# Kernel optimization log

Measured on AMD Instinct MI355X. Metric: run time of the kernel, lower is better.

## Reference

```python
import jax, jax.numpy as jnp
import numpy as np

NPX = 128      # nPxPup
FOV = 512      # fovInPixel = 2*samp*nPxPup, samp=2
NMODES = 54    # len(jModes)
BATCH = 8
ALPHA = np.pi / 2


def _make_consts():
    # circular pupil on the nPxPup grid
    x = np.linspace(-1.0, 1.0, NPX)
    X, Y = np.meshgrid(x, x)
    pupil = ((X ** 2 + Y ** 2) <= 1.0).astype(np.float32)
    # 4-faced pyramid phase mask on the FOV grid, pre-fftshifted
    f = np.arange(FOV) - FOV / 2
    FX, FY = np.meshgrid(f, f)
    pyr_phase = ALPHA * (np.abs(FX) + np.abs(FY))
    pyr_mask = np.fft.fftshift(np.exp(-1j * pyr_phase)).astype(np.complex64)
    return pupil, pyr_mask


def setup_inputs() -> dict:
    key = jax.random.key(0)
    k1, k2 = jax.random.split(key)
    pupil_np, mask_np = _make_consts()
    pupil = jnp.asarray(pupil_np)                      # [NPX,NPX] float32
    pyrMask = jnp.asarray(mask_np)                     # [FOV,FOV] complex64 (fftshifted)
    # Zernike-like mode basis restricted to the pupil, column-major modes as in the torch buffer
    modes = jax.random.normal(k1, (NPX * NPX, NMODES), dtype=jnp.float32) * pupil.reshape(-1, 1)
    OL1 = (jnp.eye(NMODES, dtype=jnp.float32) * 0.1)   # learnable parameter
    inputs = jax.random.normal(k2, (BATCH, 1, NPX, NPX), dtype=jnp.float32) * pupil
    return {"inputs": inputs, "modes": modes, "OL1": OL1, "pupil": pupil, "pyrMask": pyrMask}


def _prop(phase, pupil, pyrMask):
    """Vanilla pyramid WFS propagation (modulation=0).
    phase: [B,1,NPX,NPX] -> intensity [B,1,FOV,FOV]."""
    u = (pupil * jnp.exp(1j * phase)).astype(jnp.complex64)
    npv = (FOV - NPX) // 2
    field = jnp.zeros(phase.shape[:2] + (FOV, FOV), dtype=jnp.complex64)
    field = field.at[:, :, npv:npv + NPX, npv:npv + NPX].set(u)
    buf = jnp.fft.fft2(field) * pyrMask          # focal plane * pyramid mask
    return jnp.abs(jnp.fft.fft2(buf)) ** 2       # detector intensity


def reference(inputs, modes, OL1, pupil, pyrMask):
    n_modes = OL1.shape[0]
    optModes = modes @ OL1                                     # [NPX*NPX, M]
    # reference (flat wavefront) intensity
    flat = (jnp.ones((NPX, NPX), jnp.float32) * (pupil > 0))[None, None]
    I0 = _prop(flat, pupil, pyrMask)
    I0 = I0 / jnp.sum(I0)                                      # [1,1,FOV,FOV]
    gainRow = jnp.sum(OL1, axis=1)                             # [M]
    # batch the per-mode +/- push-pull propagations in one FFT pass
    zim = optModes.T.reshape(n_modes, 1, NPX, NPX)
    phases = jnp.concatenate([zim, -zim], axis=0)              # [2M,1,NPX,NPX]
    I4 = _prop(phases, pupil, pyrMask)
    I4 = I4 / jnp.sum(I4, axis=(1, 2, 3), keepdims=True)
    sp = I4[:n_modes] - I0
    sm = I4[n_modes:] - I0
    MZc = 0.5 * (sp - sm) / gainRow[:, None, None, None]
    IM = MZc.reshape(n_modes, -1).T                            # [FOV*FOV, M]
    CM = jnp.linalg.pinv(IM)                                   # [M, FOV*FOV]
    # measurement
    Ip = _prop(inputs, pupil, pyrMask)                         # [B,1,FOV,FOV]
    Inorm = jnp.sum(Ip, axis=(1, 2, 3), keepdims=True)
    Ip = Ip / Inorm - I0
    y = CM @ Ip.reshape(Ip.shape[0], -1).T                     # [M, B]
    return y
```

## Files before the change

kernel.cpp:

```cpp
#include <hip/hip_runtime.h>
#include <math.h>

#define NPIXK 262144
#define ROWF2 584

__device__ __forceinline__ int padi8(int i) { return i + (i >> 3); }
__device__ __forceinline__ int padi(int i) { return i + (i >> 5); }

#define WSYNC asm volatile("s_waitcnt lgkmcnt(0)" ::: "memory")

__device__ __forceinline__ float2 cmul(float2 a, float2 b) {
    return make_float2(a.x * b.x - a.y * b.y, a.x * b.y + a.y * b.x);
}

__device__ __forceinline__ void twchain(float ang, float2 tw[8]) {
    float s, c;
    sincosf(ang, &s, &c);
    float2 w1 = make_float2(c, s);
    float2 w2 = cmul(w1, w1);
    float2 w4 = cmul(w2, w2);
    tw[1] = w1;
    tw[2] = w2;
    tw[3] = cmul(w1, w2);
    tw[4] = w4;
    tw[5] = cmul(w1, w4);
    tw[6] = cmul(w2, w4);
    tw[7] = cmul(tw[3], w4);
}

__device__ __forceinline__ void fft8f(float vr[8], float vi[8]) {
    float er[4], ei[4], orr[4], oi[4];
    {
        float t0r = vr[0] + vr[4], t0i = vi[0] + vi[4];
        float t1r = vr[0] - vr[4], t1i = vi[0] - vi[4];
        float t2r = vr[2] + vr[6], t2i = vi[2] + vi[6];
        float t3r = vi[2] - vi[6], t3i = vr[6] - vr[2];
        er[0] = t0r + t2r; ei[0] = t0i + t2i;
        er[1] = t1r + t3r; ei[1] = t1i + t3i;
        er[2] = t0r - t2r; ei[2] = t0i - t2i;
        er[3] = t1r - t3r; ei[3] = t1i - t3i;
    }
    {
        float t0r = vr[1] + vr[5], t0i = vi[1] + vi[5];
        float t1r = vr[1] - vr[5], t1i = vi[1] - vi[5];
        float t2r = vr[3] + vr[7], t2i = vi[3] + vi[7];
        float t3r = vi[3] - vi[7], t3i = vr[7] - vr[3];
        orr[0] = t0r + t2r; oi[0] = t0i + t2i;
        orr[1] = t1r + t3r; oi[1] = t1i + t3i;
        orr[2] = t0r - t2r; oi[2] = t0i - t2i;
        orr[3] = t1r - t3r; oi[3] = t1i - t3i;
    }
    const float c = 0.70710678118654752440f;
    vr[0] = er[0] + orr[0]; vi[0] = ei[0] + oi[0];
    vr[4] = er[0] - orr[0]; vi[4] = ei[0] - oi[0];
    float t1r = c * (orr[1] + oi[1]), t1i = c * (oi[1] - orr[1]);
    vr[1] = er[1] + t1r; vi[1] = ei[1] + t1i;
    vr[5] = er[1] - t1r; vi[5] = ei[1] - t1i;
    float t2r = oi[2], t2i = -orr[2];
    vr[2] = er[2] + t2r; vi[2] = ei[2] + t2i;
    vr[6] = er[2] - t2r; vi[6] = ei[2] - t2i;
    float t3r = c * (oi[3] - orr[3]), t3i = -c * (orr[3] + oi[3]);
    vr[3] = er[3] + t3r; vi[3] = ei[3] + t3i;
    vr[7] = er[3] - t3r; vi[7] = ei[3] - t3i;
}

__device__ __forceinline__ void fft8_s34(float vr[8], float vi[8]) {
    const float c = 0.70710678118654752440f;
    float x3r = vr[3], x3i = vi[3], x4r = vr[4], x4i = vi[4];
    float A = c * (x3r + x3i), B = c * (x3r - x3i);
    vr[0] = x3r + x4r; vi[0] = x3i + x4i;
    vr[1] = -B - x4r;  vi[1] = -A - x4i;
    vr[2] = x4r - x3i; vi[2] = x3r + x4i;
    vr[3] = A - x4r;   vi[3] = -B - x4i;
    vr[4] = x4r - x3r; vi[4] = x4i - x3i;
    vr[5] = B - x4r;   vi[5] = A - x4i;
    vr[6] = x3i + x4r; vi[6] = x4i - x3r;
    vr[7] = -A - x4r;  vi[7] = B - x4i;
}

template <int SPARSE>
__device__ __forceinline__ void fft512v(float2* L, int t,
                                        float vr[8], float vi[8]) {
    if (SPARSE) fft8_s34(vr, vi); else fft8f(vr, vi);
    {
        float2* wb = L + 9 * t;
#pragma unroll
        for (int r = 0; r < 8; ++r) wb[r] = make_float2(vr[r], vi[r]);
    }
    float2 tw[8];
    twchain((float)(t & 7) * -0.09817477042468103870f, tw);
    WSYNC;
    {
        const float2* rb = L + t + (t >> 3);
        { float2 a = rb[0]; vr[0] = a.x; vi[0] = a.y; }
#pragma unroll
        for (int r = 1; r < 8; ++r) {
            float2 a = rb[72 * r];
            float2 w = tw[r];
            vr[r] = a.x * w.x - a.y * w.y;
            vi[r] = a.x * w.y + a.y * w.x;
        }
        fft8f(vr, vi);
        WSYNC;
        float2* wb = L + 9 * t;
#pragma unroll
        for (int r = 0; r < 8; ++r) wb[r] = make_float2(vr[r], vi[r]);
    }
    twchain((float)t * -0.01227184630308512985f, tw);
    WSYNC;
    {
        const float2* rb = L + 9 * (t & 7) + (t >> 3);
        { float2 a = rb[0]; vr[0] = a.x; vi[0] = a.y; }
#pragma unroll
        for (int r = 1; r < 8; ++r) {
            float2 a = rb[72 * r];
            float2 w = tw[r];
            vr[r] = a.x * w.x - a.y * w.y;
            vi[r] = a.x * w.y + a.y * w.x;
        }
        fft8f(vr, vi);
    }
}

#define FFT_LDS __shared__ float2 lds[4][ROWF2];

__device__ __forceinline__ double lsx(int i) {
    if (i == 127) return 1.0;
    return __dadd_rn(__dmul_rn((double)i, 2.0 / 127.0), -1.0);
}
__device__ __forceinline__ double pupilAt(int r, int c) {
    double xc = lsx(c), xr = lsx(r);
    double s = __dadd_rn(__dmul_rn(xc, xc), __dmul_rn(xr, xr));
    return (s <= 1.0) ? 1.0 : 0.0;
}

__global__ __launch_bounds__(256, 8) void k_s1(const float* __restrict__ optT,
                                               const float* __restrict__ inputs,
                                               float2* __restrict__ T1, int giBase) {
    FFT_LDS
    int tid = threadIdx.x, w = tid >> 6, t = tid & 63;
    int r = (blockIdx.x & 31) * 4 + w;
    int im = blockIdx.x >> 5;
    int gi = (giBase >= 0) ? giBase + im : ((im == 0) ? 0 : 108 + im);

    float vr[8], vi[8];
#pragma unroll
    for (int q = 0; q < 8; ++q) { vr[q] = 0.f; vi[q] = 0.f; }
#pragma unroll
    for (int h = 0; h < 2; ++h) {
        int c = t + 64 * h;
        int p = r * 128 + c;
        float pu = (float)pupilAt(r, c);
        float ph;
        if (gi == 0) {
            ph = pu;
        } else if (gi < 109) {
            ph = optT[(gi - 1) * 16384 + p];
        } else {
            ph = inputs[(gi - 109) * 16384 + p];
        }
        float s, cs; sincosf(ph, &s, &cs);
        vr[3 + h] = pu * cs; vi[3 + h] = pu * s;
    }
    fft512v<1>(lds[w], t, vr, vi);
    WSYNC;
#pragma unroll
    for (int q = 0; q < 8; ++q) {
        int d = t + 64 * q;
        lds[w][padi8(d)] = make_float2(vr[q], vi[q]);
    }
    __syncthreads();
    int r0 = (blockIdx.x & 31) * 4;
    float2* dst = T1 + (size_t)im * 65536;
#pragma unroll
    for (int it = 0; it < 8; ++it) {
        int g = it * 256 + tid;
        int l = g >> 2, rr = g & 3;
        dst[(size_t)l * 128 + r0 + rr] = lds[rr][padi8(l)];
    }
}

__global__ __launch_bounds__(256, 8) void k_s23(const float2* __restrict__ T1,
                                                float2* __restrict__ C2p) {
    FFT_LDS
    int tid = threadIdx.x, w = tid >> 6, t = tid & 63;
    int imgL = blockIdx.x >> 7, l = (blockIdx.x & 127) * 4 + w;
    const float2* src = T1 + (size_t)imgL * 65536 + (size_t)l * 128;
    float vr[8], vi[8];
#pragma unroll
    for (int q = 0; q < 8; ++q) { vr[q] = 0.f; vi[q] = 0.f; }
    float2 a0 = src[t], a1 = src[t + 64];
    vr[3] = a0.x; vi[3] = a0.y;
    vr[4] = a1.x; vi[4] = a1.y;
    fft512v<1>(lds[w], t, vr, vi);
    int gl = (l <= 256) ? l : 512 - l;
    int l0 = (blockIdx.x & 127) * 4;
#pragma unroll
    for (int q = 0; q < 8; ++q) {
        int k = t + 64 * q;
        int gk = (k <= 256) ? k : 512 - k;
        int n = (gk + gl) & 3;
        float a = vr[q], b = vi[q], X, Y;
        if (n == 0)      { X = a;  Y = b;  }
        else if (n == 1) { X = b;  Y = -a; }
        else if (n == 2) { X = -a; Y = -b; }
        else             { X = -b; Y = a;  }
        vr[q] = X; vi[q] = Y;
    }
    fft512v<0>(lds[w], t, vr, vi);
    WSYNC;
#pragma unroll
    for (int q = 0; q < 8; ++q) {
        int d = t + 64 * q;
        lds[w][padi8(d)] = make_float2(vr[q], vi[q]);
    }
    __syncthreads();
    float2* dst = C2p + (size_t)imgL * NPIXK;
#pragma unroll
    for (int it = 0; it < 8; ++it) {
        int g = it * 256 + tid;
        int p = g >> 2, rr = g & 3;
        dst[(size_t)p * 512 + l0 + rr] = lds[rr][padi8(p)];
    }
}

__global__ __launch_bounds__(256, 8) void k_s4(const float2* __restrict__ C2,
                                               float* __restrict__ dst,
                                               const float* __restrict__ I0,
                                               int ep) {
    FFT_LDS
    int tid = threadIdx.x, w = tid >> 6, t = tid & 63;
    int imgL = blockIdx.x >> 7, p = (blockIdx.x & 127) * 4 + w;
    const float2* src = C2 + (size_t)imgL * NPIXK + (size_t)p * 512;
    float vr[8], vi[8];
#pragma unroll
    for (int q = 0; q < 8; ++q) { float2 a = src[t + 64 * q]; vr[q] = a.x; vi[q] = a.y; }
    fft512v<0>(lds[w], t, vr, vi);
    size_t rowOff = (size_t)p * 512;
    float* drow = dst + (size_t)imgL * NPIXK + rowOff;
    if (ep == 0) {
#pragma unroll
        for (int q = 0; q < 8; ++q) {
            int k = t + 64 * q;
            drow[k] = vr[q] * vr[q] + vi[q] * vi[q];
        }
    } else {
#pragma unroll
        for (int q = 0; q < 8; ++q) {
            int k = t + 64 * q;
            float mag2 = vr[q] * vr[q] + vi[q] * vi[q];
            drow[k] = mag2 - I0[rowOff + k];
        }
    }
}

__global__ __launch_bounds__(256, 8) void k_s4pm(const float2* __restrict__ C2p,
                                                 float* __restrict__ dst,
                                                 const double* __restrict__ gainInv,
                                                 int gBase) {
    FFT_LDS
    int tid = threadIdx.x, w = tid >> 6, t = tid & 63;
    int imgL = blockIdx.x >> 7, q2 = blockIdx.x & 127;
    int p = 2 * q2 + (w & 1) + (w >> 1) * 256;
    const float2* src = C2p + (size_t)imgL * NPIXK + (size_t)p * 512;
    float vr[8], vi[8], m2[8];
#pragma unroll
    for (int q = 0; q < 8; ++q) { float2 a = src[t + 64 * q]; vr[q] = a.x; vi[q] = a.y; }
    fft512v<0>(lds[w], t, vr, vi);
    WSYNC;
    float* mrow = (float*)lds[w];
#pragma unroll
    for (int q = 0; q < 8; ++q) {
        m2[q] = vr[q] * vr[q] + vi[q] * vi[q];
        mrow[padi(t + 64 * q)] = m2[q];
    }
    __syncthreads();
    float g = (float)gainInv[gBase + imgL];
    float* drow = dst + (size_t)imgL * NPIXK + (size_t)p * 512;
    const float* prow = (const float*)lds[w ^ 2];
#pragma unroll
    for (int q = 0; q < 8; ++q) {
        int qp = (q + 4) & 7;
        float other = prow[padi(t + 64 * qp)];
        drow[t + 64 * q] = g * (m2[q] - other);
    }
}

__global__ __launch_bounds__(256) void k_modes(const float* __restrict__ modes,
                                               const float* __restrict__ OL1,
                                               float* __restrict__ optT,
                                               double* __restrict__ gainInv,
                                               double* __restrict__ G,
                                               double* __restrict__ bmat) {
    __shared__ float sM[64 * 54];
    __shared__ float sOL[54 * 54];
    int tid = threadIdx.x;
    if (blockIdx.x == 0) {
        for (int i = tid; i < 54 * 54; i += 256) G[i] = 0.0;
        for (int i = tid; i < 54 * 8; i += 256) bmat[i] = 0.0;
    }
    for (int i = tid; i < 54 * 54; i += 256) sOL[i] = OL1[i];
    const float* msrc = modes + (size_t)blockIdx.x * 64 * 54;
    for (int i = tid; i < 64 * 54; i += 256) sM[i] = msrc[i];
    __syncthreads();
    int pl = tid & 63, mg = tid >> 6;
    int p = blockIdx.x * 64 + pl;
    const float* mrow = sM + pl * 54;
    for (int m = mg; m < 54; m += 4) {
        double acc = 0.0;
#pragma unroll
        for (int j = 0; j < 54; ++j)
            acc += (double)mrow[j] * (double)sOL[j * 54 + m];
        optT[(size_t)m * 16384 + p] = (float)acc;
    }
    if (blockIdx.x == 0 && tid < 54) {
        double g = 0.0;
        for (int j = 0; j < 54; ++j) g += (double)sOL[tid * 54 + j];
        gainInv[tid] = 0.5 / g;
    }
}

__device__ __forceinline__ float dot4(float4 a, float4 b) {
    return a.x * b.x + a.y * b.y + a.z * b.z + a.w * b.w;
}

__global__ __launch_bounds__(256) void k_gram(const float* __restrict__ Mz,
                                              const float* __restrict__ V,
                                              const float* __restrict__ I0,
                                              float* __restrict__ part,
                                              int cA, int PROWS, int subI0) {
    __shared__ float Ms[54 * 128];
    __shared__ float Vs[8 * 128];
    int tid = threadIdx.x;
    int cQ = (cA + 3) >> 2;
    int nQT = cQ * (cQ + 1) / 2;
    int nT = nQT + cQ * 8;
    int task = tid;
    int kind = (task < nQT) ? 0 : (task < nT ? 1 : 2);
    int r0[4], r1[4], bb = 0, Ti = 0, Tj = 0, Qi = 0;
    if (kind == 0) {
        int rem = task;
        while (rem >= cQ - Ti) { rem -= cQ - Ti; ++Ti; }
        Tj = Ti + rem;
#pragma unroll
        for (int q = 0; q < 4; ++q) {
            int i = 4 * Ti + q; r0[q] = (i < cA) ? i : cA - 1;
            int j = 4 * Tj + q; r1[q] = (j < cA) ? j : cA - 1;
        }
    } else if (kind == 1) {
        int tb = task - nQT;
        Qi = tb >> 3; bb = tb & 7;
#pragma unroll
        for (int q = 0; q < 4; ++q) {
            int i = 4 * Qi + q; r0[q] = (i < cA) ? i : cA - 1;
        }
    }
    float s[16];
#pragma unroll
    for (int q = 0; q < 16; ++q) s[q] = 0.f;

    size_t P0 = (size_t)blockIdx.x * 128;
    for (int idx = tid; idx < cA * 32; idx += 256) {
        int i = idx >> 5, v4 = idx & 31;
        ((float4*)Ms)[i * 32 + v4] =
            *(const float4*)(Mz + (size_t)i * NPIXK + P0 + v4 * 4);
    }
    for (int idx = tid; idx < 8 * 32; idx += 256) {
        int b = idx >> 5, v4 = idx & 31;
        float4 vv = *(const float4*)(V + (size_t)b * NPIXK + P0 + v4 * 4);
        if (subI0) {
            float4 i0 = *(const float4*)(I0 + P0 + v4 * 4);
            vv.x -= i0.x; vv.y -= i0.y; vv.z -= i0.z; vv.w -= i0.w;
        }
        ((float4*)Vs)[b * 32 + v4] = vv;
    }
    __syncthreads();
    if (kind == 0) {
        for (int kk = 0; kk < 32; ++kk) {
            int pp = (kk + tid) & 31;
            float4 a0 = ((float4*)(Ms + r0[0] * 128))[pp];
            float4 a1 = ((float4*)(Ms + r0[1] * 128))[pp];
            float4 a2 = ((float4*)(Ms + r0[2] * 128))[pp];
            float4 a3 = ((float4*)(Ms + r0[3] * 128))[pp];
            float4 b0 = ((float4*)(Ms + r1[0] * 128))[pp];
            float4 b1 = ((float4*)(Ms + r1[1] * 128))[pp];
            float4 b2 = ((float4*)(Ms + r1[2] * 128))[pp];
            float4 b3 = ((float4*)(Ms + r1[3] * 128))[pp];
            s[0] += dot4(a0, b0); s[1] += dot4(a0, b1);
            s[2] += dot4(a0, b2); s[3] += dot4(a0, b3);
            s[4] += dot4(a1, b0); s[5] += dot4(a1, b1);
            s[6] += dot4(a1, b2); s[7] += dot4(a1, b3);
            s[8] += dot4(a2, b0); s[9] += dot4(a2, b1);
            s[10] += dot4(a2, b2); s[11] += dot4(a2, b3);
            s[12] += dot4(a3, b0); s[13] += dot4(a3, b1);
            s[14] += dot4(a3, b2); s[15] += dot4(a3, b3);
        }
    } else if (kind == 1) {
        for (int kk = 0; kk < 32; ++kk) {
            int pp = (kk + tid) & 31;
            float4 vb = ((float4*)Vs)[bb * 32 + pp];
            float4 a0 = ((float4*)(Ms + r0[0] * 128))[pp];
            float4 a1 = ((float4*)(Ms + r0[1] * 128))[pp];
            float4 a2 = ((float4*)(Ms + r0[2] * 128))[pp];
            float4 a3 = ((float4*)(Ms + r0[3] * 128))[pp];
            s[0] += dot4(a0, vb); s[1] += dot4(a1, vb);
            s[2] += dot4(a2, vb); s[3] += dot4(a3, vb);
        }
    }
    float* dst = part + (size_t)blockIdx.x * PROWS;
    if (kind == 0) {
#pragma unroll
        for (int q = 0; q < 16; ++q) dst[task * 16 + q] = s[q];
    } else if (kind == 1) {
#pragma unroll
        for (int q = 0; q < 4; ++q)
            dst[nQT * 16 + (task - nQT) * 4 + q] = s[q];
    }
}

__global__ __launch_bounds__(256) void k_gred3(const float* __restrict__ part,
                                               double* __restrict__ G,
                                               double* __restrict__ bmat,
                                               int cA, int m0, int PROWS) {
    __shared__ double red[8][33];
    int tid = threadIdx.x;
    int r = tid & 31, grp = tid >> 5;
    int row = blockIdx.x * 32 + r;
    int bid0 = blockIdx.y * 256;
    double acc = 0.0;
    if (row < PROWS)
        for (int k = 0; k < 32; ++k)
            acc += (double)part[(size_t)(bid0 + grp + 8 * k) * PROWS + row];
    red[grp][r] = acc;
    __syncthreads();
    if (tid < 32) {
        int rr = blockIdx.x * 32 + tid;
        if (rr < PROWS) {
            double s = 0.0;
#pragma unroll
            for (int g = 0; g < 8; ++g) s += red[g][tid];
            int cQ = (cA + 3) >> 2;
            int nQT = cQ * (cQ + 1) / 2;
            if (rr < nQT * 16) {
                int tile = rr >> 4, q = rr & 15;
                int Ti = 0, rem = tile;
                while (rem >= cQ - Ti) { rem -= cQ - Ti; ++Ti; }
                int Tj = Ti + rem;
                int i = 4 * Ti + (q >> 2), j = 4 * Tj + (q & 3);
                if (i < cA && j < cA && i <= j)
                    atomicAdd(&G[(m0 + i) * 54 + (m0 + j)], s);
            } else {
                int qb = rr - nQT * 16;
                int tb = qb >> 2, qq = qb & 3;
                int Qi = tb >> 3, bbb = tb & 7;
                int i = 4 * Qi + qq;
                if (i < cA) atomicAdd(&bmat[(m0 + i) * 8 + bbb], s);
            }
        }
    }
}

__global__ __launch_bounds__(256) void k_gramx(const float* __restrict__ MzA,
                                               const float* __restrict__ MzB,
                                               double* __restrict__ G,
                                               int cA, int m0, int mb) {
    __shared__ float Ms[54 * 128];
    __shared__ float Bs[128];
    int tid = threadIdx.x;
    double acc = 0.0;
    for (int ch = 0; ch < 4; ++ch) {
        size_t P0 = (size_t)blockIdx.x * 512 + (size_t)ch * 128;
        __syncthreads();
        for (int idx = tid; idx < cA * 32; idx += 256) {
            int i = idx >> 5, v4 = idx & 31;
            ((float4*)Ms)[i * 32 + v4] =
                *(const float4*)(MzA + (size_t)i * NPIXK + P0 + v4 * 4);
        }
        if (tid < 128) Bs[tid] = MzB[P0 + tid];
        __syncthreads();
        if (tid < cA) {
            const float* ri = Ms + tid * 128;
            float s = 0.f;
            for (int k = 0; k < 128; ++k) {
                int p = (k + tid) & 127;
                s += ri[p] * Bs[p];
            }
            acc += (double)s;
        }
    }
    if (tid < cA) atomicAdd(&G[(m0 + tid) * 54 + mb], acc);
}

__global__ __launch_bounds__(512) void k_solve(const double* __restrict__ G,
                                               const double* __restrict__ bmat,
                                               float* __restrict__ out) {
    __shared__ double A[54][65];
    int tid = threadIdx.x;
    int r = tid >> 3, cg = tid & 7;
    for (int idx = tid; idx < 54 * 62; idx += 512) {
        int i = idx / 62, c = idx % 62;
        A[i][c] = (c < 54) ? ((i <= c) ? G[i * 54 + c] : G[c * 54 + i])
                           : bmat[i * 8 + (c - 54)];
    }
    __syncthreads();
    for (int p = 0; p < 54; ++p) {
        double f = 0.0;
        bool act = (r < 54) && (r != p);
        if (act) f = A[r][p] / A[p][p];
        __syncthreads();
        if (act) {
#pragma unroll
            for (int k = 0; k < 8; ++k) {
                int c = cg + 8 * k;
                if (c < 62) A[r][c] -= f * A[p][c];
            }
        }
        __syncthreads();
    }
    for (int idx = tid; idx < 54 * 8; idx += 512) {
        int m = idx >> 3, b = idx & 7;
        out[idx] = (float)(A[m][54 + b] / A[m][m]);
    }
}

__global__ void k_zero(float* out, int n) {
    int i = blockIdx.x * 256 + threadIdx.x;
    if (i < n) out[i] = 0.f;
}

extern "C" void kernel_launch(void* const* d_in, const int* in_sizes, int n_in,
                              void* d_out, int out_size, void* d_ws, size_t ws_size,
                              hipStream_t stream) {
    float* out = (float*)d_out;
    if (out_size <= 0) return;
    if (n_in < 3 || in_sizes[0] != 131072 || in_sizes[1] != 884736 ||
        in_sizes[2] != 2916 || out_size < 432) {
        k_zero<<<(out_size + 255) / 256, 256, 0, stream>>>(out, out_size);
        return;
    }
    const float* inputs = (const float*)d_in[0];
    const float* modes  = (const float*)d_in[1];
    const float* OL1    = (const float*)d_in[2];

    char* ws = (char*)d_ws;
    size_t off = 0;
    auto alloc = [&](size_t bytes) -> void* {
        void* p = ws + off;
        off += (bytes + 255) & ~(size_t)255;
        return p;
    };
    float*  optT    = (float*)  alloc((size_t)54 * 16384 * 4);
    double* gainInv = (double*) alloc(64 * 8);
    double* G       = (double*) alloc(54 * 54 * 8);
    double* bmat    = (double*) alloc(54 * 8 * 8);
    float*  I0buf   = (float*)  alloc((size_t)9 * NPIXK * 4);
    float*  V       = I0buf + NPIXK;
    float*  MzB1    = (float*)  alloc((size_t)NPIXK * 4);
    float*  part    = (float*)  alloc((size_t)2048 * 2128 * 4);

    const size_t IMG  = (size_t)NPIXK * 4 + 256;
    const size_t PIPE = ((size_t)65536 * 8 + 256) + ((size_t)NPIXK * 8 + 256);
    size_t rem = (ws_size > off + 4096) ? ws_size - off - 4096 : 0;
    int cA, chunkP;
    if (rem >= 54 * IMG + PIPE) {
        cA = 54;
        size_t c = (rem - 54 * IMG) / PIPE;
        chunkP = (c > 54) ? 54 : (int)c;
        if (chunkP < 1) chunkP = 1;
    } else if (rem >= IMG + PIPE) {
        cA = (int)((rem - PIPE) / IMG);
        if (cA > 53) cA = 53;
        if (cA < 1) cA = 1;
        size_t left = rem - (size_t)cA * IMG;
        chunkP = (int)(left / PIPE);
        if (chunkP < 1) chunkP = 1;
        if (chunkP > cA) chunkP = cA;
    } else {
        k_zero<<<(out_size + 255) / 256, 256, 0, stream>>>(out, out_size);
        return;
    }
    float*  MzA = (float*)  alloc((size_t)cA * NPIXK * 4);
    float2* T1  = (float2*) alloc((size_t)chunkP * 65536 * 8);
    float2* C2p = (float2*) alloc((size_t)chunkP * NPIXK * 8);
    if (off > ws_size) {
        k_zero<<<(out_size + 255) / 256, 256, 0, stream>>>(out, out_size);
        return;
    }

    auto prop_one = [&](int giBase, int n, float* dst, int ep) {
        for (int s = 0; s < n; s += chunkP) {
            int nn = n - s; if (nn > chunkP) nn = chunkP;
            k_s1<<<nn * 32, 256, 0, stream>>>(optT, inputs, T1, giBase + s);
            k_s23<<<nn * 128, 256, 0, stream>>>(T1, C2p);
            k_s4<<<nn * 128, 256, 0, stream>>>(C2p, dst + (size_t)s * NPIXK,
                                               I0buf, ep);
        }
    };
    auto prop_pm = [&](int m0, int n, float* dst, int gBase) {
        for (int s = 0; s < n; s += chunkP) {
            int nn = n - s; if (nn > chunkP) nn = chunkP;
            k_s1<<<nn * 32, 256, 0, stream>>>(optT, inputs, T1, 1 + m0 + s);
            k_s23<<<nn * 128, 256, 0, stream>>>(T1, C2p);
            k_s4pm<<<nn * 128, 256, 0, stream>>>(C2p,
                                                 dst + (size_t)s * NPIXK,
                                                 gainInv, gBase + s);
        }
    };

    k_modes<<<256, 256, 0, stream>>>(modes, OL1, optT, gainInv, G, bmat);
    int subI0;
    if (chunkP >= 9) {
        k_s1<<<9 * 32, 256, 0, stream>>>(optT, inputs, T1, -1);
        k_s23<<<9 * 128, 256, 0, stream>>>(T1, C2p);
        k_s4<<<9 * 128, 256, 0, stream>>>(C2p, I0buf, I0buf, 0);
        subI0 = 1;
    } else {
        prop_one(0, 1, I0buf, 0);
        prop_one(109, 8, V, 2);
        subI0 = 0;
    }
    for (int m0 = 0; m0 < 54; m0 += cA) {
        int ca = 54 - m0; if (ca > cA) ca = cA;
        prop_pm(m0, ca, MzA, m0);
        int cQ = (ca + 3) >> 2;
        int PROWS = cQ * (cQ + 1) / 2 * 16 + cQ * 32;
        k_gram<<<2048, 256, 0, stream>>>(MzA, V, I0buf, part, ca, PROWS, subI0);
        k_gred3<<<dim3((PROWS + 31) / 32, 8), 256, 0, stream>>>(part, G, bmat,
                                                                ca, m0, PROWS);
        for (int mb = m0 + ca; mb < 54; ++mb) {
            prop_pm(mb, 1, MzB1, mb);
            k_gramx<<<512, 256, 0, stream>>>(MzA, MzB1, G, ca, m0, mb);
        }
    }
    k_solve<<<1, 512, 0, stream>>>(G, bmat, out);
}
```

Before: 290.4 us.

## Add specialized 8x8-register-tiled Gram kernel for the full 54-mode case

Adds k_gram54, which computes the 62x62 Gram matrix (54 modes plus 8 measurement vectors) over 128-pixel slices, using 8x8 register tiles per thread with threads split across k-segments. Partial sums are reduced within the block through shared memory, then across blocks in a new double-precision reduction kernel that scatters results into G and bmat. It runs only when the workspace can hold all 54 mode images; otherwise the old chunked path is used. The 64-float accumulator raises register pressure, and the fixed task-to-thread mapping leaves some threads idle.

Measured after the change: 414.5 us. +42.7%, slower.

```diff
diff --git a/kernel.cpp b/kernel.cpp
--- a/kernel.cpp
+++ b/kernel.cpp
@@ -322,6 +322,123 @@
 
 __device__ __forceinline__ float dot4(float4 a, float4 b) {
     return a.x * b.x + a.y * b.y + a.z * b.z + a.w * b.w;
+}
+
+#define GPROWS 2304
+__global__ __launch_bounds__(256, 4) void k_gram54(const float* __restrict__ Mz,
+                                                   const float* __restrict__ V,
+                                                   const float* __restrict__ I0,
+                                                   float* __restrict__ part,
+                                                   int subI0) {
+    __shared__ float Ms[64 * 128];
+    int tid = threadIdx.x;
+    size_t P0 = (size_t)blockIdx.x * 128;
+    for (int idx = tid; idx < 64 * 32; idx += 256) {
+        int i = idx >> 5, v4 = idx & 31;
+        float4 vv;
+        if (i < 54) {
+            vv = *(const float4*)(Mz + (size_t)i * NPIXK + P0 + v4 * 4);
+        } else if (i < 62) {
+            vv = *(const float4*)(V + (size_t)(i - 54) * NPIXK + P0 + v4 * 4);
+            if (subI0) {
+                float4 i0 = *(const float4*)(I0 + P0 + v4 * 4);
+                vv.x -= i0.x; vv.y -= i0.y; vv.z -= i0.z; vv.w -= i0.w;
+            }
+        } else {
+            vv = make_float4(0.f, 0.f, 0.f, 0.f);
+        }
+        ((float4*)Ms)[i * 32 + v4] = vv;
+    }
+    int task = tid / 7, sl = tid - task * 7;
+    if (task > 35) task = 35;
+    int oi = 0, rem = task;
+    while (rem >= 8 - oi) { rem -= 8 - oi; ++oi; }
+    int oj = oi + rem;
+    int ra = 8 * oi, rb = 8 * oj;
+    int start = (32 * sl) / 7, len = (32 * (sl + 1)) / 7 - start;
+    int rot = tid % len;
+    float s[64];
+#pragma unroll
+    for (int q = 0; q < 64; ++q) s[q] = 0.f;
+    __syncthreads();
+#pragma unroll 1
+    for (int k = 0; k < 5; ++k) {
+        if (k < len) {
+            int kk = k + rot; if (kk >= len) kk -= len;
+            int pp = start + kk;
+            float4 b[8];
+#pragma unroll
+            for (int j = 0; j < 8; ++j)
+                b[j] = ((const float4*)Ms)[(rb + j) * 32 + pp];
+#pragma unroll
+            for (int i = 0; i < 8; ++i) {
+                float4 a = ((const float4*)Ms)[(ra + i) * 32 + pp];
+#pragma unroll
+                for (int j = 0; j < 8; ++j) {
+                    float acc = s[i * 8 + j];
+                    acc = fmaf(a.x, b[j].x, acc);
+                    acc = fmaf(a.y, b[j].y, acc);
+                    acc = fmaf(a.z, b[j].z, acc);
+                    acc = fmaf(a.w, b[j].w, acc);
+                    s[i * 8 + j] = acc;
+                }
+            }
+        }
+    }
+    float* red = Ms;
+    float* dst = part + (size_t)blockIdx.x * GPROWS;
+#pragma unroll 1
+    for (int c = 0; c < 4; ++c) {
+        __syncthreads();
+        if (tid < 252) {
+#pragma unroll
+            for (int q = 0; q < 4; ++q)
+                ((float4*)(red + tid * 16))[q] =
+                    make_float4(s[c * 16 + 4 * q], s[c * 16 + 4 * q + 1],
+                                s[c * 16 + 4 * q + 2], s[c * 16 + 4 * q + 3]);
+        }
+        __syncthreads();
+        for (int idx = tid; idx < 576; idx += 256) {
+            int tk = idx >> 4, j = idx & 15;
+            float acc = 0.f;
+#pragma unroll
+            for (int ss = 0; ss < 7; ++ss) acc += red[(tk * 7 + ss) * 16 + j];
+            dst[tk * 64 + c * 16 + j] = acc;
+        }
+    }
+}
+
+__global__ __launch_bounds__(256) void k_gred54(const float* __restrict__ part,
+                                                double* __restrict__ G,
+                                                double* __restrict__ bmat) {
+    __shared__ double red[8][33];
+    int tid = threadIdx.x;
+    int r = tid & 31, grp = tid >> 5;
+    int row = blockIdx.x * 32 + r;
+    int bid0 = blockIdx.y * 256;
+    double acc = 0.0;
+    for (int k = 0; k < 32; ++k)
+        acc += (double)part[(size_t)(bid0 + grp + 8 * k) * GPROWS + row];
+    red[grp][r] = acc;
+    __syncthreads();
+    if (tid < 32) {
+        int rr = blockIdx.x * 32 + tid;
+        double s = 0.0;
+#pragma unroll
+        for (int g = 0; g < 8; ++g) s += red[g][tid];
+        int tk = rr >> 6, q = rr & 63;
+        int oi = 0, rem = tk;
+        while (rem >= 8 - oi) { rem -= 8 - oi; ++oi; }
+        int oj = oi + rem;
+        int a = 8 * oi + (q >> 3), b = 8 * oj + (q & 7);
+        if (a < 54) {
+            if (b < 54) {
+                if (a <= b) atomicAdd(&G[a * 54 + b], s);
+            } else if (b < 62) {
+                atomicAdd(&bmat[a * 8 + (b - 54)], s);
+            }
+        }
+    }
 }
 
 __global__ __launch_bounds__(256) void k_gram(const float* __restrict__ Mz,
@@ -556,7 +673,7 @@
     float*  I0buf   = (float*)  alloc((size_t)9 * NPIXK * 4);
     float*  V       = I0buf + NPIXK;
     float*  MzB1    = (float*)  alloc((size_t)NPIXK * 4);
-    float*  part    = (float*)  alloc((size_t)2048 * 2128 * 4);
+    float*  part    = (float*)  alloc((size_t)2048 * GPROWS * 4);
 
     const size_t IMG  = (size_t)NPIXK * 4 + 256;
     const size_t PIPE = ((size_t)65536 * 8 + 256) + ((size_t)NPIXK * 8 + 256);
@@ -619,17 +736,23 @@
         prop_one(109, 8, V, 2);
         subI0 = 0;
     }
-    for (int m0 = 0; m0 < 54; m0 += cA) {
-        int ca = 54 - m0; if (ca > cA) ca = cA;
-        prop_pm(m0, ca, MzA, m0);
-        int cQ = (ca + 3) >> 2;
-        int PROWS = cQ * (cQ + 1) / 2 * 16 + cQ * 32;
-        k_gram<<<2048, 256, 0, stream>>>(MzA, V, I0buf, part, ca, PROWS, subI0);
-        k_gred3<<<dim3((PROWS + 31) / 32, 8), 256, 0, stream>>>(part, G, bmat,
-                                                                ca, m0, PROWS);
-        for (int mb = m0 + ca; mb < 54; ++mb) {
-            prop_pm(mb, 1, MzB1, mb);
-            k_gramx<<<512, 256, 0, stream>>>(MzA, MzB1, G, ca, m0, mb);
+    if (cA >= 54) {
+        prop_pm(0, 54, MzA, 0);
+        k_gram54<<<2048, 256, 0, stream>>>(MzA, V, I0buf, part, subI0);
+        k_gred54<<<dim3(72, 8), 256, 0, stream>>>(part, G, bmat);
+    } else {
+        for (int m0 = 0; m0 < 54; m0 += cA) {
+            int ca = 54 - m0; if (ca > cA) ca = cA;
+            prop_pm(m0, ca, MzA, m0);
+            int cQ = (ca + 3) >> 2;
+            int PROWS = cQ * (cQ + 1) / 2 * 16 + cQ * 32;
+            k_gram<<<2048, 256, 0, stream>>>(MzA, V, I0buf, part, ca, PROWS, subI0);
+            k_gred3<<<dim3((PROWS + 31) / 32, 8), 256, 0, stream>>>(part, G, bmat,
+                                                                    ca, m0, PROWS);
+            for (int mb = m0 + ca; mb < 54; ++mb) {
+                prop_pm(mb, 1, MzB1, mb);
+                k_gramx<<<512, 256, 0, stream>>>(MzA, MzB1, G, ca, m0, mb);
+            }
         }
     }
     k_solve<<<1, 512, 0, stream>>>(G, bmat, out);
```
